# Optimization experiments

Measured on AMD Instinct MI355X. Metric: run time of the kernel, lower is better.

Reference implementation:

```python
import jax, jax.numpy as jnp
import numpy as np

X_DIM = 512
Y_DIM = 512
HID = 300
N = 2048


def setup_inputs() -> dict:
    key = jax.random.key(0)
    ks = jax.random.split(key, 8)
    scale = 0.05
    return {
        "pos_local": jax.random.normal(ks[0], (N, X_DIM), jnp.float32),
        "pos_global": jax.random.normal(ks[1], (N, Y_DIM), jnp.float32),
        "neg_local": jax.random.normal(ks[2], (N, X_DIM), jnp.float32),
        "neg_global": jax.random.normal(ks[3], (N, Y_DIM), jnp.float32),
        "W1": jax.random.normal(ks[4], (X_DIM + Y_DIM, HID), jnp.float32) * scale,
        "b1": jnp.zeros((HID,), jnp.float32),
        "W2": jax.random.normal(ks[5], (HID, 1), jnp.float32) * scale,
        "b2": jnp.zeros((1,), jnp.float32),
        "batch_size": 256,
    }


def reference(pos_local, pos_global, neg_local, neg_global, W1, b1, W2, b2, batch_size):
    # Split first-layer weight into local/global halves so we never materialize
    # the concatenated pair tensor: F(cat(l, g)) uses l @ W1l + g @ W1g.
    W1l, W1g = W1[:X_DIM], W1[X_DIM:]
    w2, bias2 = W2[:, 0], b2[0]

    # Positive branch: plain batched MLP, chunking does not change the math.
    h0 = jax.nn.relu(pos_local @ W1l + pos_global @ W1g + b1)  # [N, HID]
    t0 = jax.nn.softplus(h0 @ w2 + bias2).mean()

    # Negative branch: per chunk of size B, pair (local_j, global_i),
    # score[i, j] = F(local_j, global_i); logsumexp over j, mean over i.
    nc = neg_local.shape[0] // batch_size
    nl = neg_local.reshape(nc, batch_size, X_DIM)
    ng = neg_global.reshape(nc, batch_size, Y_DIM)

    def chunk_term(carry, lg):
        l, g = lg                                   # [B, x], [B, y]
        lp = l @ W1l                                # [B, HID]
        gp = g @ W1g                                # [B, HID]
        h = jax.nn.relu(gp[:, None, :] + lp[None, :, :] + b1)  # [B, B, HID]
        s = jax.nn.softplus(h @ w2 + bias2)         # [B, B]
        val = jax.scipy.special.logsumexp(s, axis=1).mean()
        return carry + val, None

    total, _ = jax.lax.scan(chunk_term, jnp.float32(0.0), (nl, ng))
    t1 = total / nc

    lower_bound = t0 - t1
    return -lower_bound
```

## Files before the change

kernel.cpp:

```cpp
#include <hip/hip_runtime.h>
#include <math.h>

#define NR   2048
#define XD   512
#define HID  300
#define BS   256
#define NPAD 320
#define KTOT 1024
#define GSTR 304
#define HSTR 304
#define KP   320
#define NNEG 256

typedef __attribute__((ext_vector_type(8))) short bf16x8;
typedef __attribute__((ext_vector_type(4))) float f32x4;

__device__ __forceinline__ float softplus_f(float x) {
    return fmaxf(x, 0.f) + log1pf(__expf(-fabsf(x)));
}
__device__ __forceinline__ unsigned short f2bf(float f) {
    unsigned int u = __float_as_uint(f);
    u += 0x7FFFu + ((u >> 16) & 1u);
    return (unsigned short)(u >> 16);
}
__device__ __forceinline__ float bf2f(unsigned short h) {
    return __uint_as_float((unsigned int)h << 16);
}
__device__ __forceinline__ void unpk(unsigned int u, float& lo, float& hi) {
    lo = __uint_as_float(u << 16);
    hi = __uint_as_float(u & 0xFFFF0000u);
}

__global__ __launch_bounds__(256) void convert(
    const float* __restrict__ pl, const float* __restrict__ pg,
    const float* __restrict__ nl, const float* __restrict__ ng,
    const float* __restrict__ W1,
    unsigned short* __restrict__ Aneg, unsigned short* __restrict__ Apos,
    unsigned short* __restrict__ Wt, unsigned int* __restrict__ counter)
{
    const int b = blockIdx.x, tid = threadIdx.x;
    if (b == 0 && tid == 0) *counter = 0u;
    if (b < 4096) {
        const int m = (b < 2048) ? b : b - 2048;
        const float* lo = (b < 2048) ? nl : pl;
        const float* hi = (b < 2048) ? ng : pg;
        unsigned short* dst = (b < 2048) ? Aneg : Apos;
        const int kq = tid * 4;
        const float4 v = (kq < XD) ? *(const float4*)(lo + m * XD + kq)
                                   : *(const float4*)(hi + m * XD + kq - XD);
        ushort4 o;
        o.x = f2bf(v.x); o.y = f2bf(v.y); o.z = f2bf(v.z); o.w = f2bf(v.w);
        *(ushort4*)(dst + m * KTOT + kq) = o;
    } else {
        __shared__ unsigned short ts[16][72];
        const int t = b - 4096;
        const int nt = t % 20, kt = t / 20;
        const int n = nt * 16 + (tid & 15);
        const int kl = tid >> 4;
        #pragma unroll
        for (int j = 0; j < 4; ++j) {
            const int k = kt * 64 + kl * 4 + j;
            ts[tid & 15][kl * 4 + j] = f2bf((n < HID) ? W1[k * HID + n] : 0.f);
        }
        __syncthreads();
        const int nw = tid >> 4, kw = (tid & 15) * 4;
        ushort4 o;
        o.x = ts[nw][kw]; o.y = ts[nw][kw + 1]; o.z = ts[nw][kw + 2]; o.w = ts[nw][kw + 3];
        *(ushort4*)(Wt + (nt * 16 + nw) * KTOT + kt * 64 + kw) = o;
    }
}

__global__ __launch_bounds__(64) void mfma_gemm(
    const unsigned short* __restrict__ Aneg, const unsigned short* __restrict__ Apos,
    const unsigned short* __restrict__ Wt, const float* __restrict__ b1,
    unsigned short* __restrict__ LP4h, unsigned short* __restrict__ GPBh,
    float* __restrict__ P0a, float* __restrict__ P0b)
{
    const int bid = blockIdx.x;
    const int job = bid / 320, t = bid % 320;
    const int m0 = (t & 63) * 32, n0 = (t >> 6) * 64;
    const int lane = threadIdx.x;
    const int r = lane & 15, g = lane >> 4;

    const unsigned short* A = (job >= 2) ? Apos : Aneg;
    const int kbeg = (job & 1) ? XD : 0;

    const unsigned short* ap[2];
    const unsigned short* bp[4];
    #pragma unroll
    for (int mi = 0; mi < 2; ++mi)
        ap[mi] = A + (m0 + 16 * mi + r) * KTOT + kbeg + 8 * g;
    #pragma unroll
    for (int ni = 0; ni < 4; ++ni)
        bp[ni] = Wt + (n0 + 16 * ni + r) * KTOT + kbeg + 8 * g;

    f32x4 acc[2][4] = {};

    #pragma unroll 8
    for (int k = 0; k < XD; k += 32) {
        bf16x8 a[2], w[4];
        #pragma unroll
        for (int mi = 0; mi < 2; ++mi) a[mi] = *(const bf16x8*)(ap[mi] + k);
        #pragma unroll
        for (int ni = 0; ni < 4; ++ni) w[ni] = *(const bf16x8*)(bp[ni] + k);
        #pragma unroll
        for (int mi = 0; mi < 2; ++mi)
            #pragma unroll
            for (int ni = 0; ni < 4; ++ni)
                acc[mi][ni] = __builtin_amdgcn_mfma_f32_16x16x32_bf16(
                    a[mi], w[ni], acc[mi][ni], 0, 0, 0);
    }

    #pragma unroll
    for (int mi = 0; mi < 2; ++mi) {
        #pragma unroll
        for (int ni = 0; ni < 4; ++ni) {
            const int n = n0 + ni * 16 + r;
            const int mb = m0 + mi * 16 + 4 * g;
            const f32x4 v = acc[mi][ni];
            if (job == 0) {
                unsigned short* base = LP4h + ((size_t)(n >> 3) * NR + mb) * 8 + (n & 7);
                base[0]  = f2bf(v[0]); base[8]  = f2bf(v[1]);
                base[16] = f2bf(v[2]); base[24] = f2bf(v[3]);
            } else if (n < HID) {
                if (job == 1) {
                    const float bias = b1[n];
                    #pragma unroll
                    for (int j = 0; j < 4; ++j)
                        GPBh[(size_t)(mb + j) * HSTR + n] = f2bf(v[j] + bias);
                } else {
                    float* out = (job == 2) ? P0a : P0b;
                    #pragma unroll
                    for (int j = 0; j < 4; ++j)
                        out[(size_t)(mb + j) * GSTR + n] = v[j];
                }
            }
        }
    }
}

__global__ __launch_bounds__(512, 2) void negpos(
    const unsigned short* __restrict__ LP4h, const unsigned short* __restrict__ GPBh,
    const float* __restrict__ P0a, const float* __restrict__ P0b,
    const float* __restrict__ b1, const float* __restrict__ W2,
    const float* __restrict__ b2,
    float* __restrict__ negE, float* __restrict__ posP,
    unsigned int* __restrict__ counter, float* __restrict__ out)
{
    __shared__ __align__(16) float w2s[KP];
    __shared__ __align__(16) float gbs[8][KP];
    __shared__ __align__(16) float pacc[8][BS][8];
    __shared__ float sC[8];
    __shared__ float red[4][8];
    __shared__ float redp[8];
    __shared__ int sh_last;
    const int tid = threadIdx.x, bid = blockIdx.x;
    const int kh = tid >> 6, lh = tid & 63;
    const float b2v = b2[0];
    const int chunk = bid >> 5, g0 = (bid & 31) * 8;
    const size_t cb = (size_t)chunk * BS;

    const unsigned short* gpb = GPBh + (cb + g0) * HSTR;
    if (tid < KP) {
        const bool v = tid < HID;
        w2s[tid] = v ? 0.5f * W2[tid] : 0.f;
        #pragma unroll
        for (int g = 0; g < 8; ++g)
            gbs[g][tid] = v ? bf2f(gpb[g * HSTR + tid]) : 0.f;
    }
    __syncthreads();

    {
        float c = 0.f;
        #pragma unroll
        for (int h = 0; h < 2; ++h) {
            const int k4 = lh + 64 * h;
            if (k4 < 80) {
                const float4 g4 = *(const float4*)&gbs[kh][k4 * 4];
                const float4 w4 = *(const float4*)&w2s[k4 * 4];
                c += g4.x * w4.x + g4.y * w4.y + g4.z * w4.z + g4.w * w4.w;
            }
        }
        #pragma unroll
        for (int o = 32; o > 0; o >>= 1) c += __shfl_xor(c, o);
        if (lh == 0) sC[kh] = c;
    }

    float acc[8][4];
    float q[4] = {0.f, 0.f, 0.f, 0.f};
    #pragma unroll
    for (int gt = 0; gt < 8; ++gt)
        #pragma unroll
        for (int j = 0; j < 4; ++j) acc[gt][j] = 0.f;

    #pragma unroll
    for (int i = 0; i < 5; ++i) {
        const int k8 = 5 * kh + i;
        uint4 u0 = *(const uint4*)(LP4h + ((size_t)k8 * NR + cb + lh)       * 8);
        uint4 u1 = *(const uint4*)(LP4h + ((size_t)k8 * NR + cb + lh + 64)  * 8);
        uint4 u2 = *(const uint4*)(LP4h + ((size_t)k8 * NR + cb + lh + 128) * 8);
        uint4 u3 = *(const uint4*)(LP4h + ((size_t)k8 * NR + cb + lh + 192) * 8);
        const float4 wa = *(const float4*)&w2s[k8 * 8];
        const float4 wb = *(const float4*)&w2s[k8 * 8 + 4];
        float fv[4][8];
        unpk(u0.x, fv[0][0], fv[0][1]); unpk(u0.y, fv[0][2], fv[0][3]);
        unpk(u0.z, fv[0][4], fv[0][5]); unpk(u0.w, fv[0][6], fv[0][7]);
        unpk(u1.x, fv[1][0], fv[1][1]); unpk(u1.y, fv[1][2], fv[1][3]);
        unpk(u1.z, fv[1][4], fv[1][5]); unpk(u1.w, fv[1][6], fv[1][7]);
        unpk(u2.x, fv[2][0], fv[2][1]); unpk(u2.y, fv[2][2], fv[2][3]);
        unpk(u2.z, fv[2][4], fv[2][5]); unpk(u2.w, fv[2][6], fv[2][7]);
        unpk(u3.x, fv[3][0], fv[3][1]); unpk(u3.y, fv[3][2], fv[3][3]);
        unpk(u3.z, fv[3][4], fv[3][5]); unpk(u3.w, fv[3][6], fv[3][7]);
        #pragma unroll
        for (int j = 0; j < 4; ++j) {
            q[j] = fmaf(wa.x, fv[j][0], q[j]); q[j] = fmaf(wa.y, fv[j][1], q[j]);
            q[j] = fmaf(wa.z, fv[j][2], q[j]); q[j] = fmaf(wa.w, fv[j][3], q[j]);
            q[j] = fmaf(wb.x, fv[j][4], q[j]); q[j] = fmaf(wb.y, fv[j][5], q[j]);
            q[j] = fmaf(wb.z, fv[j][6], q[j]); q[j] = fmaf(wb.w, fv[j][7], q[j]);
        }
        #pragma unroll
        for (int gt = 0; gt < 8; ++gt) {
            const float4 ga = *(const float4*)&gbs[gt][k8 * 8];
            const float4 gb = *(const float4*)&gbs[gt][k8 * 8 + 4];
            #pragma unroll
            for (int j = 0; j < 4; ++j) {
                acc[gt][j] = fmaf(fabsf(ga.x + fv[j][0]), wa.x, acc[gt][j]);
                acc[gt][j] = fmaf(fabsf(ga.y + fv[j][1]), wa.y, acc[gt][j]);
                acc[gt][j] = fmaf(fabsf(ga.z + fv[j][2]), wa.z, acc[gt][j]);
                acc[gt][j] = fmaf(fabsf(ga.w + fv[j][3]), wa.w, acc[gt][j]);
                acc[gt][j] = fmaf(fabsf(gb.x + fv[j][4]), wb.x, acc[gt][j]);
                acc[gt][j] = fmaf(fabsf(gb.y + fv[j][5]), wb.y, acc[gt][j]);
                acc[gt][j] = fmaf(fabsf(gb.z + fv[j][6]), wb.z, acc[gt][j]);
                acc[gt][j] = fmaf(fabsf(gb.w + fv[j][7]), wb.w, acc[gt][j]);
            }
        }
    }

    #pragma unroll
    for (int j = 0; j < 4; ++j) {
        *(float4*)&pacc[kh][lh + 64 * j][0] =
            make_float4(acc[0][j] + q[j], acc[1][j] + q[j],
                        acc[2][j] + q[j], acc[3][j] + q[j]);
        *(float4*)&pacc[kh][lh + 64 * j][4] =
            make_float4(acc[4][j] + q[j], acc[5][j] + q[j],
                        acc[6][j] + q[j], acc[7][j] + q[j]);
    }
    __syncthreads();

    if (tid < 256) {
        float s[8];
        #pragma unroll
        for (int gt = 0; gt < 8; ++gt) s[gt] = sC[gt];
        #pragma unroll
        for (int k = 0; k < 8; ++k) {
            const float4 p0 = *(const float4*)&pacc[k][tid][0];
            const float4 p1 = *(const float4*)&pacc[k][tid][4];
            s[0] += p0.x; s[1] += p0.y; s[2] += p0.z; s[3] += p0.w;
            s[4] += p1.x; s[5] += p1.y; s[6] += p1.z; s[7] += p1.w;
        }
        const int wid = tid >> 6;
        #pragma unroll
        for (int gt = 0; gt < 8; ++gt) {
            float v = __expf(softplus_f(s[gt] + b2v));
            #pragma unroll
            for (int o = 32; o > 0; o >>= 1) v += __shfl_xor(v, o);
            if ((tid & 63) == 0) red[wid][gt] = v;
        }
    }
    __syncthreads();
    if (tid == 0) {
        #pragma unroll
        for (int gt = 0; gt < 8; ++gt)
            negE[bid * 8 + gt] = red[0][gt] + red[1][gt] + red[2][gt] + red[3][gt];
    }

    {
        const int row = bid * 8 + kh;
        const float4* ra = (const float4*)(P0a + (size_t)row * GSTR);
        const float4* rb = (const float4*)(P0b + (size_t)row * GSTR);
        float d = 0.f;
        #pragma unroll
        for (int h = 0; h < 2; ++h) {
            const int k4 = lh + 64 * h;
            if (k4 < 75) {
                const float4 aa = ra[k4], bb4 = rb[k4];
                const float4 bb = *(const float4*)(b1 + k4 * 4);
                const float4 wv = *(const float4*)(W2 + k4 * 4);
                d += fmaxf(aa.x + bb4.x + bb.x, 0.f) * wv.x
                   + fmaxf(aa.y + bb4.y + bb.y, 0.f) * wv.y
                   + fmaxf(aa.z + bb4.z + bb.z, 0.f) * wv.z
                   + fmaxf(aa.w + bb4.w + bb.w, 0.f) * wv.w;
            }
        }
        #pragma unroll
        for (int o = 32; o > 0; o >>= 1) d += __shfl_xor(d, o);
        if (lh == 0) redp[kh] = softplus_f(d + b2v);
    }
    __syncthreads();

    if (tid == 0) {
        posP[bid] = redp[0] + redp[1] + redp[2] + redp[3]
                  + redp[4] + redp[5] + redp[6] + redp[7];
        __threadfence();
        const unsigned t = atomicAdd(counter, 1u);
        sh_last = (t == NNEG - 1) ? 1 : 0;
    }
    __syncthreads();
    if (sh_last) {
        __threadfence();
        const volatile float* ne = (const volatile float*)negE;
        const volatile float* pp = (const volatile float*)posP;
        float v = 0.f;
        for (int i = tid; i < 2048; i += 512)
            v += __logf(ne[i]);
        if (tid < NNEG) v -= pp[tid];
        #pragma unroll
        for (int o = 32; o > 0; o >>= 1) v += __shfl_xor(v, o);
        if (lh == 0) redp[kh] = v;
        __syncthreads();
        if (tid == 0)
            out[0] = (redp[0] + redp[1] + redp[2] + redp[3]
                    + redp[4] + redp[5] + redp[6] + redp[7]) * (1.f / 2048.f);
    }
}

extern "C" void kernel_launch(void* const* d_in, const int* in_sizes, int n_in,
                              void* d_out, int out_size, void* d_ws, size_t ws_size,
                              hipStream_t stream)
{
    const float* pl = (const float*)d_in[0];
    const float* pg = (const float*)d_in[1];
    const float* nl = (const float*)d_in[2];
    const float* ng = (const float*)d_in[3];
    const float* W1 = (const float*)d_in[4];
    const float* b1 = (const float*)d_in[5];
    const float* W2 = (const float*)d_in[6];
    const float* b2 = (const float*)d_in[7];

    char* ws = (char*)d_ws;
    unsigned short* Aneg = (unsigned short*)(ws);
    unsigned short* Apos = (unsigned short*)(ws + (4u << 20));
    unsigned short* Wt   = (unsigned short*)(ws + (8u << 20));
    unsigned short* LP4h = (unsigned short*)(ws + (9u << 20));
    unsigned short* GPBh = (unsigned short*)(ws + (11u << 20));
    float* P0a  = (float*)(ws + (13u << 20));
    float* P0b  = (float*)(ws + (16u << 20));
    float* negE = (float*)(ws + (19u << 20));
    float* posP = negE + 2048;
    unsigned int* counter = (unsigned int*)(ws + (19u << 20) + 65536);
    float* out  = (float*)d_out;

    hipLaunchKernelGGL(convert, dim3(4096 + 320), dim3(256), 0, stream,
                       pl, pg, nl, ng, W1, Aneg, Apos, Wt, counter);
    hipLaunchKernelGGL(mfma_gemm, dim3(1280), dim3(64), 0, stream,
                       Aneg, Apos, Wt, b1, LP4h, GPBh, P0a, P0b);
    hipLaunchKernelGGL(negpos, dim3(NNEG), dim3(512), 0, stream,
                       LP4h, GPBh, P0a, P0b, b1, W2, b2, negE, posP, counter, out);
}
```

Measured before the change: 59.21 us.

## Stage GEMM tiles through LDS with double-buffered direct global-to-LDS loads

The projection GEMM changes from single-wave blocks that read bf16 operands straight from global memory to 256-thread blocks computing a 128x64 tile. Each K=64 slice of A and W is staged into padded LDS buffers with global_load_lds, double-buffered so the next slice's loads overlap the current MFMAs. This aims to cut redundant global and L2 traffic through tile reuse across waves. In exchange it launches fewer blocks, adds barriers and LDS use, and relies on the LDS-DMA wait semantics being right.

```diff
diff --git a/kernel.cpp b/kernel.cpp
--- a/kernel.cpp
+++ b/kernel.cpp
@@ -11,6 +11,11 @@
 #define HSTR 304
 #define KP   320
 #define NNEG 256
+#define BM   128
+#define BN   64
+#define BK   64
+#define LDA  72
+#define NGB  320
 
 typedef __attribute__((ext_vector_type(8))) short bf16x8;
 typedef __attribute__((ext_vector_type(4))) float f32x4;
@@ -29,6 +34,11 @@
 __device__ __forceinline__ void unpk(unsigned int u, float& lo, float& hi) {
     lo = __uint_as_float(u << 16);
     hi = __uint_as_float(u & 0xFFFF0000u);
+}
+__device__ __forceinline__ void gload_lds16(const void* g, void* l) {
+    __builtin_amdgcn_global_load_lds(
+        (const __attribute__((address_space(1))) void*)g,
+        (__attribute__((address_space(3))) void*)l, 16, 0, 0);
 }
 
 __global__ __launch_bounds__(256) void convert(
@@ -70,45 +80,72 @@
     }
 }
 
-__global__ __launch_bounds__(64) void mfma_gemm(
+__global__ __launch_bounds__(256, 2) void mfma_gemm(
     const unsigned short* __restrict__ Aneg, const unsigned short* __restrict__ Apos,
     const unsigned short* __restrict__ Wt, const float* __restrict__ b1,
     unsigned short* __restrict__ LP4h, unsigned short* __restrict__ GPBh,
     float* __restrict__ P0a, float* __restrict__ P0b)
 {
+    __shared__ __align__(16) unsigned short As[2][BM * LDA];
+    __shared__ __align__(16) unsigned short Ws[2][BN * LDA];
     const int bid = blockIdx.x;
-    const int job = bid / 320, t = bid % 320;
-    const int m0 = (t & 63) * 32, n0 = (t >> 6) * 64;
-    const int lane = threadIdx.x;
+    const int job = bid / 80, t = bid % 80;
+    const int m0 = (t / 5) * BM, n0 = (t % 5) * BN;
+    const int tid = threadIdx.x;
+    const int w = tid >> 6, lane = tid & 63;
     const int r = lane & 15, g = lane >> 4;
 
     const unsigned short* A = (job >= 2) ? Apos : Aneg;
     const int kbeg = (job & 1) ? XD : 0;
 
-    const unsigned short* ap[2];
-    const unsigned short* bp[4];
-    #pragma unroll
-    for (int mi = 0; mi < 2; ++mi)
-        ap[mi] = A + (m0 + 16 * mi + r) * KTOT + kbeg + 8 * g;
-    #pragma unroll
-    for (int ni = 0; ni < 4; ++ni)
-        bp[ni] = Wt + (n0 + 16 * ni + r) * KTOT + kbeg + 8 * g;
+    auto stage = [&](int buf, int kc) {
+        #pragma unroll
+        for (int i = 0; i < 5; ++i) {
+            const int d = i * 256 + tid;
+            if (d < BM * 9) {
+                const int row = d / 9, c = d % 9;
+                const int sk = (c < 8) ? c * 8 : 0;
+                gload_lds16(A + (size_t)(m0 + row) * KTOT + kbeg + kc + sk,
+                            &As[buf][(size_t)d * 8]);
+            }
+        }
+        #pragma unroll
+        for (int i = 0; i < 3; ++i) {
+            const int d = i * 256 + tid;
+            if (d < BN * 9) {
+                const int row = d / 9, c = d % 9;
+                const int sk = (c < 8) ? c * 8 : 0;
+                gload_lds16(Wt + (size_t)(n0 + row) * KTOT + kbeg + kc + sk,
+                            &Ws[buf][(size_t)d * 8]);
+            }
+        }
+    };
 
     f32x4 acc[2][4] = {};
 
-    #pragma unroll 8
-    for (int k = 0; k < XD; k += 32) {
-        bf16x8 a[2], w[4];
-        #pragma unroll
-        for (int mi = 0; mi < 2; ++mi) a[mi] = *(const bf16x8*)(ap[mi] + k);
-        #pragma unroll
-        for (int ni = 0; ni < 4; ++ni) w[ni] = *(const bf16x8*)(bp[ni] + k);
-        #pragma unroll
-        for (int mi = 0; mi < 2; ++mi)
+    stage(0, 0);
+    __syncthreads();
+
+    for (int kc = 0; kc < 8; ++kc) {
+        const int cur = kc & 1;
+        if (kc < 7) stage(cur ^ 1, (kc + 1) * BK);
+        #pragma unroll
+        for (int ks = 0; ks < 2; ++ks) {
+            bf16x8 a[2], wv[4];
+            #pragma unroll
+            for (int mi = 0; mi < 2; ++mi)
+                a[mi] = *(const bf16x8*)&As[cur][(w * 32 + mi * 16 + r) * LDA + ks * 32 + g * 8];
             #pragma unroll
             for (int ni = 0; ni < 4; ++ni)
-                acc[mi][ni] = __builtin_amdgcn_mfma_f32_16x16x32_bf16(
-                    a[mi], w[ni], acc[mi][ni], 0, 0, 0);
+                wv[ni] = *(const bf16x8*)&Ws[cur][(ni * 16 + r) * LDA + ks * 32 + g * 8];
+            #pragma unroll
+            for (int mi = 0; mi < 2; ++mi)
+                #pragma unroll
+                for (int ni = 0; ni < 4; ++ni)
+                    acc[mi][ni] = __builtin_amdgcn_mfma_f32_16x16x32_bf16(
+                        a[mi], wv[ni], acc[mi][ni], 0, 0, 0);
+        }
+        __syncthreads();
     }
 
     #pragma unroll
@@ -116,7 +153,7 @@
         #pragma unroll
         for (int ni = 0; ni < 4; ++ni) {
             const int n = n0 + ni * 16 + r;
-            const int mb = m0 + mi * 16 + 4 * g;
+            const int mb = m0 + w * 32 + mi * 16 + 4 * g;
             const f32x4 v = acc[mi][ni];
             if (job == 0) {
                 unsigned short* base = LP4h + ((size_t)(n >> 3) * NR + mb) * 8 + (n & 7);
@@ -352,7 +389,7 @@
 
     hipLaunchKernelGGL(convert, dim3(4096 + 320), dim3(256), 0, stream,
                        pl, pg, nl, ng, W1, Aneg, Apos, Wt, counter);
-    hipLaunchKernelGGL(mfma_gemm, dim3(1280), dim3(64), 0, stream,
+    hipLaunchKernelGGL(mfma_gemm, dim3(NGB), dim3(256), 0, stream,
                        Aneg, Apos, Wt, b1, LP4h, GPBh, P0a, P0b);
     hipLaunchKernelGGL(negpos, dim3(NNEG), dim3(512), 0, stream,
                        LP4h, GPBh, P0a, P0b, b1, W2, b2, negE, posP, counter, out);
```

Result: faster. 54.01 us (median of 2 runs) (-8.8%).
